# Performance work log

Measured on AMD Instinct MI355X. Metric: run time of the kernel, lower is better.

## Reference

```python
import jax, jax.numpy as jnp
import numpy as np

PI = np.float32(np.pi)

def _sinc_tf_style(x):
    # Faithful to the TF code: replace x==0 by 1.0 BEFORE sin(pi*x)/(pi*x).
    x = jnp.where(x == 0, jnp.float32(1.0), x)
    pix = PI * x
    return jnp.sin(pix) / pix

def setup_inputs() -> dict:
    key = jax.random.key(0)
    k1, k2 = jax.random.split(key)
    B, H, W, C = 2, 256, 256, 2
    img = jax.random.normal(k1, (B, H, W, C), dtype=jnp.float32)
    fmap = jax.random.normal(k2, (B, H, W, C), dtype=jnp.float32)  # flow along H
    return {"img": img, "fmap": fmap}

def reference(img, fmap):
    # img, fmap: [B, H, W, C]; 1D sinc-kernel warp along axis 1 (H).
    B, H, W, C = img.shape
    j = jnp.arange(H, dtype=jnp.float32)
    # source coordinate for each input row i: i_x[b,i,w,c] = clip(f + i, 0, H-1)
    i_x = jnp.clip(fmap + j[None, :, None, None], 0.0, jnp.float32(H - 1))
    # Kf[b,i,j,w,c] = sinc(i_x[b,i,w,c] - j)   -> [B, H, H, W, C]
    diff = i_x[:, :, None, :, :] - j[None, None, :, None, None]
    Kf = _sinc_tf_style(diff)
    # out[b,j,w,c] = sum_i img[b,i,w,c] * Kf[b,i,j,w,c]
    out = jnp.einsum('biwc,bijwc->bjwc', img, Kf)
    return out
```

## Files before the change

### kernel.cpp

```cpp
#include <hip/hip_runtime.h>
#include <cmath>

constexpr int Bn = 2, Hn = 256, Wn = 256, Cn = 2;
constexpr int NG = 16;
constexpr int NJ = 4;

__global__ __launch_bounds__(1024, 4) void sinc_main_kernel(
    const float* __restrict__ img, const float* __restrict__ fmap,
    float* __restrict__ out)
{
    const float INV_PI = 0x1.45f306p-2f;

    __shared__ __align__(16) float sh_x[Cn][Hn];
    __shared__ __align__(16) float sh_p[Cn][Hn];
    __shared__ float sh_acc[NG][Hn * Cn];

    const int bw = blockIdx.x;
    const int b  = bw >> 8;
    const int w  = bw & 255;
    const int t  = threadIdx.x;

    if (t < Hn * Cn) {
        const int i = t & 255, c = t >> 8;
        const size_t off = (((size_t)b * Hn + i) * Wn + w) * Cn + c;
        const float f = fmap[off];
        float x0 = fminf(fmaxf(f + (float)i, 0.0f), 255.0f);
        const float n = rintf(x0);
        const float r = x0 - n;
        float sp = __builtin_amdgcn_sinf(0.5f * r) * INV_PI;
        if (((int)n) & 1) sp = -sp;
        const float p = img[off] * sp;
        if (p == 0.0f) x0 += 0x1p-15f;
        sh_x[c][i] = x0;
        sh_p[c][i] = p;
    }
    __syncthreads();

    const int ig = t >> 6;
    const int jl = t & 63;

    float acc[NJ][2];
#pragma unroll
    for (int jj = 0; jj < NJ; ++jj) { acc[jj][0] = 0.0f; acc[jj][1] = 0.0f; }

    const float4* qx = (const float4*)sh_x;
    const float4* qp = (const float4*)sh_p;

#pragma unroll
    for (int q = 0; q < 4; ++q) {
        const int iq = ig * 4 + q;
        const float4 x0q = qx[iq],      p0q = qp[iq];
        const float4 x1q = qx[64 + iq], p1q = qp[64 + iq];
#pragma unroll
        for (int jj = 0; jj < NJ; ++jj) {
            const float J = (float)(jl + 64 * jj);
            {
                const float d0 = x0q.x - J, d1 = x0q.y - J;
                const float d2 = x0q.z - J, d3 = x0q.w - J;
                const float m01 = d0 * d1, m23 = d2 * d3;
                const float n01 = fmaf(p0q.x, d1, p0q.y * d0);
                const float n23 = fmaf(p0q.z, d3, p0q.w * d2);
                const float Nv  = fmaf(n01, m23, n23 * m01);
                const float Dv  = m01 * m23;
                acc[jj][0] = fmaf(Nv, __builtin_amdgcn_rcpf(Dv), acc[jj][0]);
            }
            {
                const float d0 = x1q.x - J, d1 = x1q.y - J;
                const float d2 = x1q.z - J, d3 = x1q.w - J;
                const float m01 = d0 * d1, m23 = d2 * d3;
                const float n01 = fmaf(p1q.x, d1, p1q.y * d0);
                const float n23 = fmaf(p1q.z, d3, p1q.w * d2);
                const float Nv  = fmaf(n01, m23, n23 * m01);
                const float Dv  = m01 * m23;
                acc[jj][1] = fmaf(Nv, __builtin_amdgcn_rcpf(Dv), acc[jj][1]);
            }
        }
    }

#pragma unroll
    for (int jj = 0; jj < NJ; ++jj) {
        const int j = jl + 64 * jj;
        *(float2*)&sh_acc[ig][j * 2] = make_float2(acc[jj][0], acc[jj][1]);
    }
    __syncthreads();

    if (t < Hn * Cn) {
        float a = 0.0f;
#pragma unroll
        for (int g = 0; g < NG; ++g) a += sh_acc[g][t];
        const int j = t >> 1, c = t & 1;
        const float sgn = (j & 1) ? -1.0f : 1.0f;
        out[(((size_t)b * Hn + j) * Wn + w) * Cn + c] = sgn * a;
    }
}

extern "C" void kernel_launch(void* const* d_in, const int* in_sizes, int n_in,
                              void* d_out, int out_size, void* d_ws, size_t ws_size,
                              hipStream_t stream)
{
    (void)in_sizes; (void)n_in; (void)out_size; (void)d_ws; (void)ws_size;
    const float* img  = (const float*)d_in[0];
    const float* fmap = (const float*)d_in[1];
    float* out = (float*)d_out;
    sinc_main_kernel<<<Bn * Wn, 1024, 0, stream>>>(img, fmap, out);
}
```

Baseline: 15.96 us.

## Process two width columns per block to double per-thread work and halve blocks

Each block now handles two adjacent w columns (four w,c streams) instead of one, so the grid halves and every thread computes 4x4 accumulators per loaded i-quad instead of 4x2. Global loads and stores become contiguous across 4 floats, the preprocessing uses all 1024 threads, and the J-subtraction work is amortised over more streams. The cross-group reduction now goes through 8 shared rows plus a two-phase add, which costs an extra barrier. The larger register footprint may reduce occupancy, and with half as many blocks the GPU may be less evenly filled.

```diff
diff --git a/kernel.cpp b/kernel.cpp
--- a/kernel.cpp
+++ b/kernel.cpp
@@ -2,8 +2,6 @@
 #include <cmath>
 
 constexpr int Bn = 2, Hn = 256, Wn = 256, Cn = 2;
-constexpr int NG = 16;
-constexpr int NJ = 4;
 
 __global__ __launch_bounds__(1024, 4) void sinc_main_kernel(
     const float* __restrict__ img, const float* __restrict__ fmap,
@@ -11,18 +9,17 @@
 {
     const float INV_PI = 0x1.45f306p-2f;
 
-    __shared__ __align__(16) float sh_x[Cn][Hn];
-    __shared__ __align__(16) float sh_p[Cn][Hn];
-    __shared__ float sh_acc[NG][Hn * Cn];
+    __shared__ __align__(16) float sh_x[4][Hn];
+    __shared__ __align__(16) float sh_p[4][Hn];
+    __shared__ __align__(16) float sh_acc[8][Hn * 4];
 
-    const int bw = blockIdx.x;
-    const int b  = bw >> 8;
-    const int w  = bw & 255;
+    const int b  = blockIdx.x >> 7;
+    const int w0 = (blockIdx.x & 127) * 2;
     const int t  = threadIdx.x;
 
-    if (t < Hn * Cn) {
-        const int i = t & 255, c = t >> 8;
-        const size_t off = (((size_t)b * Hn + i) * Wn + w) * Cn + c;
+    {
+        const int i = t >> 2, q = t & 3;
+        const size_t off = ((size_t)b * Hn + i) * (Wn * Cn) + w0 * 2 + q;
         const float f = fmap[off];
         float x0 = fminf(fmaxf(f + (float)i, 0.0f), 255.0f);
         const float n = rintf(x0);
@@ -31,66 +28,74 @@
         if (((int)n) & 1) sp = -sp;
         const float p = img[off] * sp;
         if (p == 0.0f) x0 += 0x1p-15f;
-        sh_x[c][i] = x0;
-        sh_p[c][i] = p;
+        sh_x[q][i] = x0;
+        sh_p[q][i] = p;
     }
     __syncthreads();
 
     const int ig = t >> 6;
     const int jl = t & 63;
 
-    float acc[NJ][2];
+    float acc[4][4];
 #pragma unroll
-    for (int jj = 0; jj < NJ; ++jj) { acc[jj][0] = 0.0f; acc[jj][1] = 0.0f; }
+    for (int jj = 0; jj < 4; ++jj)
+#pragma unroll
+        for (int wq = 0; wq < 4; ++wq) acc[jj][wq] = 0.0f;
 
     const float4* qx = (const float4*)sh_x;
     const float4* qp = (const float4*)sh_p;
 
 #pragma unroll
-    for (int q = 0; q < 4; ++q) {
-        const int iq = ig * 4 + q;
-        const float4 x0q = qx[iq],      p0q = qp[iq];
-        const float4 x1q = qx[64 + iq], p1q = qp[64 + iq];
+    for (int qd = 0; qd < 4; ++qd) {
+        const int iq = ig * 4 + qd;
+        float4 xv[4], pv[4];
 #pragma unroll
-        for (int jj = 0; jj < NJ; ++jj) {
+        for (int wq = 0; wq < 4; ++wq) {
+            xv[wq] = qx[wq * 64 + iq];
+            pv[wq] = qp[wq * 64 + iq];
+        }
+#pragma unroll
+        for (int jj = 0; jj < 4; ++jj) {
             const float J = (float)(jl + 64 * jj);
-            {
-                const float d0 = x0q.x - J, d1 = x0q.y - J;
-                const float d2 = x0q.z - J, d3 = x0q.w - J;
+#pragma unroll
+            for (int wq = 0; wq < 4; ++wq) {
+                const float d0 = xv[wq].x - J, d1 = xv[wq].y - J;
+                const float d2 = xv[wq].z - J, d3 = xv[wq].w - J;
                 const float m01 = d0 * d1, m23 = d2 * d3;
-                const float n01 = fmaf(p0q.x, d1, p0q.y * d0);
-                const float n23 = fmaf(p0q.z, d3, p0q.w * d2);
+                const float n01 = fmaf(pv[wq].x, d1, pv[wq].y * d0);
+                const float n23 = fmaf(pv[wq].z, d3, pv[wq].w * d2);
                 const float Nv  = fmaf(n01, m23, n23 * m01);
                 const float Dv  = m01 * m23;
-                acc[jj][0] = fmaf(Nv, __builtin_amdgcn_rcpf(Dv), acc[jj][0]);
-            }
-            {
-                const float d0 = x1q.x - J, d1 = x1q.y - J;
-                const float d2 = x1q.z - J, d3 = x1q.w - J;
-                const float m01 = d0 * d1, m23 = d2 * d3;
-                const float n01 = fmaf(p1q.x, d1, p1q.y * d0);
-                const float n23 = fmaf(p1q.z, d3, p1q.w * d2);
-                const float Nv  = fmaf(n01, m23, n23 * m01);
-                const float Dv  = m01 * m23;
-                acc[jj][1] = fmaf(Nv, __builtin_amdgcn_rcpf(Dv), acc[jj][1]);
+                acc[jj][wq] = fmaf(Nv, __builtin_amdgcn_rcpf(Dv), acc[jj][wq]);
             }
         }
     }
 
+    if (ig >= 8) {
 #pragma unroll
-    for (int jj = 0; jj < NJ; ++jj) {
-        const int j = jl + 64 * jj;
-        *(float2*)&sh_acc[ig][j * 2] = make_float2(acc[jj][0], acc[jj][1]);
+        for (int jj = 0; jj < 4; ++jj)
+            *(float4*)&sh_acc[ig - 8][(jl + 64 * jj) * 4] = *(const float4*)acc[jj];
+    }
+    __syncthreads();
+    if (ig < 8) {
+#pragma unroll
+        for (int jj = 0; jj < 4; ++jj) {
+            float4* s = (float4*)&sh_acc[ig][(jl + 64 * jj) * 4];
+            float4 v = *s;
+            v.x += acc[jj][0]; v.y += acc[jj][1];
+            v.z += acc[jj][2]; v.w += acc[jj][3];
+            *s = v;
+        }
     }
     __syncthreads();
 
-    if (t < Hn * Cn) {
+    {
         float a = 0.0f;
 #pragma unroll
-        for (int g = 0; g < NG; ++g) a += sh_acc[g][t];
-        const int j = t >> 1, c = t & 1;
+        for (int g = 0; g < 8; ++g) a += sh_acc[g][t];
+        const int j = t >> 2;
         const float sgn = (j & 1) ? -1.0f : 1.0f;
-        out[(((size_t)b * Hn + j) * Wn + w) * Cn + c] = sgn * a;
+        out[((size_t)b * Hn + j) * (Wn * Cn) + w0 * 2 + (t & 3)] = sgn * a;
     }
 }
 
@@ -102,5 +107,5 @@
     const float* img  = (const float*)d_in[0];
     const float* fmap = (const float*)d_in[1];
     float* out = (float*)d_out;
-    sinc_main_kernel<<<Bn * Wn, 1024, 0, stream>>>(img, fmap, out);
+    sinc_main_kernel<<<Bn * (Wn / 2), 1024, 0, stream>>>(img, fmap, out);
 }
```

Result: slower. 37.40 us (+134.4%).
